# Optimization experiments

Hardware: AMD Instinct MI355X
Metric: run time of the kernel (lower is better)

Reference implementation:

```python
import jax, jax.numpy as jnp
import numpy as np

N = 2048
D = 1024
H = 16
DK = D // H
TOPK = 128
LN_EPS = 1e-5


def setup_inputs() -> dict:
    key = jax.random.key(0)
    ks = jax.random.split(key, 16)
    s = 1.0 / np.sqrt(D)
    sh = 1.0 / np.sqrt(H)
    return {
        "x": jax.random.normal(ks[0], (N, D), jnp.float32),
        "Wq": jax.random.normal(ks[1], (D, D), jnp.float32) * s,
        "bq": jnp.zeros((D,), jnp.float32),
        "Wk": jax.random.normal(ks[2], (D, D), jnp.float32) * s,
        "bk": jnp.zeros((D,), jnp.float32),
        "Wv": jax.random.normal(ks[3], (D, D), jnp.float32) * s,
        "bv": jnp.zeros((D,), jnp.float32),
        "Wpre": jax.random.normal(ks[4], (H, H), jnp.float32) * sh,
        "bpre": jnp.zeros((H,), jnp.float32),
        "Wpost": jax.random.normal(ks[5], (H, H), jnp.float32) * sh,
        "bpost": jnp.zeros((H,), jnp.float32),
        "Wo": jax.random.normal(ks[6], (D, D), jnp.float32) * s,
        "bo": jnp.zeros((D,), jnp.float32),
        "gamma": jnp.ones((D,), jnp.float32),
        "beta": jnp.zeros((D,), jnp.float32),
    }


def _layernorm(x, gamma, beta):
    mu = jnp.mean(x, axis=-1, keepdims=True)
    var = jnp.var(x, axis=-1, keepdims=True)
    return (x - mu) * jax.lax.rsqrt(var + LN_EPS) * gamma + beta


def reference(x, Wq, bq, Wk, bk, Wv, bv, Wpre, bpre, Wpost, bpost, Wo, bo, gamma, beta):
    n, d = x.shape
    residual = x
    xn = _layernorm(x, gamma, beta)
    # projections -> (n, H, dk)
    q = (xn @ Wq.T + bq).reshape(n, H, DK)
    k = (xn @ Wk.T + bk).reshape(n, H, DK)
    v = (xn @ Wv.T + bv).reshape(n, H, DK)
    scale = 1.0 / np.sqrt(float(DK))
    # full scores (H, n, n); torch chunking over q is math-equivalent (dropout=0)
    scores = jnp.einsum('qhd,khd->hqk', q, k) * scale
    # pre-softmax talking heads: mix over head axis (nn.Linear on last dim h)
    scores = jnp.einsum('hqk,gh->gqk', scores, Wpre) + bpre[:, None, None]
    attn = jax.nn.softmax(scores, axis=-1)
    # top-k sparsify + renormalize (threshold mask == torch scatter mask for distinct values)
    kth = jax.lax.top_k(attn, TOPK)[0][..., -1:]
    attn = jnp.where(attn >= kth, attn, 0.0)
    attn = attn / (jnp.sum(attn, axis=-1, keepdims=True) + 1e-9)
    # post-softmax talking heads
    attn = jnp.einsum('hqk,gh->gqk', attn, Wpost) + bpost[:, None, None]
    out = jnp.einsum('hqk,khd->qhd', attn, v).reshape(n, d)
    return residual + out @ Wo.T + bo
```

## Files before the change

### kernel.cpp

```cpp
#include <hip/hip_runtime.h>
#include <stdint.h>

typedef unsigned short u16;
using bf16x8 = __attribute__((ext_vector_type(8))) short;
using f32x4  = __attribute__((ext_vector_type(4))) float;

#define N_TOK 2048
#define DMODEL 1024
#define NHEAD 16
#define HDK 64
#define TOPK_K 128

__device__ __forceinline__ u16 f2b(float f) {
  unsigned u = __float_as_uint(f);
  return (u16)((u + 0x7FFFu + ((u >> 16) & 1u)) >> 16);
}
__device__ __forceinline__ float b2f(u16 b) {
  return __uint_as_float(((unsigned)b) << 16);
}
__device__ __forceinline__ float wave_reduce_sum(float v) {
#pragma unroll
  for (int d = 32; d >= 1; d >>= 1) v += __shfl_xor(v, d);
  return v;
}
__device__ __forceinline__ unsigned bits2key(unsigned u) {
  return (u & 0x80000000u) ? ~u : (u | 0x80000000u);
}
__device__ __forceinline__ float key2f(unsigned k) {
  unsigned u = (k & 0x80000000u) ? (k ^ 0x80000000u) : ~k;
  return __uint_as_float(u);
}

__global__ __launch_bounds__(256) void ln_kernel(const float* __restrict__ x,
                                                 const float* __restrict__ gamma,
                                                 const float* __restrict__ beta,
                                                 u16* __restrict__ xn) {
  int w = threadIdx.x >> 6, lane = threadIdx.x & 63;
  int row = blockIdx.x * 4 + w;
  const float4* xr = (const float4*)(x + (size_t)row * DMODEL);
  float4 v[4];
  float s = 0.f, ss = 0.f;
#pragma unroll
  for (int i = 0; i < 4; ++i) {
    v[i] = xr[i * 64 + lane];
    s += v[i].x + v[i].y + v[i].z + v[i].w;
    ss += v[i].x * v[i].x + v[i].y * v[i].y + v[i].z * v[i].z + v[i].w * v[i].w;
  }
  s = wave_reduce_sum(s);
  ss = wave_reduce_sum(ss);
  float mu = s * (1.f / DMODEL);
  float var = ss * (1.f / DMODEL) - mu * mu;
  float rstd = rsqrtf(var + 1e-5f);
  const float4* g4 = (const float4*)gamma;
  const float4* b4 = (const float4*)beta;
  u16* xo = xn + (size_t)row * DMODEL;
#pragma unroll
  for (int i = 0; i < 4; ++i) {
    float4 g = g4[i * 64 + lane], b = b4[i * 64 + lane];
    float ox = (v[i].x - mu) * rstd * g.x + b.x;
    float oy = (v[i].y - mu) * rstd * g.y + b.y;
    float oz = (v[i].z - mu) * rstd * g.z + b.z;
    float ow = (v[i].w - mu) * rstd * g.w + b.w;
    unsigned lo = (unsigned)f2b(ox) | ((unsigned)f2b(oy) << 16);
    unsigned hi = (unsigned)f2b(oz) | ((unsigned)f2b(ow) << 16);
    *(uint2*)&xo[(i * 64 + lane) * 4] = make_uint2(lo, hi);
  }
}

__global__ __launch_bounds__(256) void cast_kernel(const float* __restrict__ in,
                                                   u16* __restrict__ out, int n8) {
  int i = blockIdx.x * 256 + threadIdx.x;
  if (i >= n8) return;
  const float4* p = (const float4*)in + (size_t)i * 2;
  float4 a = p[0], b = p[1];
  unsigned w0 = (unsigned)f2b(a.x) | ((unsigned)f2b(a.y) << 16);
  unsigned w1 = (unsigned)f2b(a.z) | ((unsigned)f2b(a.w) << 16);
  unsigned w2 = (unsigned)f2b(b.x) | ((unsigned)f2b(b.y) << 16);
  unsigned w3 = (unsigned)f2b(b.z) | ((unsigned)f2b(b.w) << 16);
  *(uint4*)&out[(size_t)i * 8] = make_uint4(w0, w1, w2, w3);
}

__global__ __launch_bounds__(256) void concat3_kernel(const float* __restrict__ a,
                                                      const float* __restrict__ b,
                                                      const float* __restrict__ c,
                                                      float* __restrict__ out) {
  int i = blockIdx.x * 256 + threadIdx.x;
  if (i < 1024) out[i] = a[i];
  else if (i < 2048) out[i] = b[i - 1024];
  else if (i < 3072) out[i] = c[i - 2048];
}

__global__ __launch_bounds__(256) void transpose_kernel(const u16* __restrict__ V, int ldv,
                                                        u16* __restrict__ Vt) {
  __shared__ u16 tile[64][72];
  int kb = blockIdx.x * 64, cb = blockIdx.y * 64;
  int t = threadIdx.x;
  int r = t >> 2, cg = (t & 3) * 16;
  *(uint4*)&tile[r][cg]     = *(const uint4*)&V[(size_t)(kb + r) * ldv + cb + cg];
  *(uint4*)&tile[r][cg + 8] = *(const uint4*)&V[(size_t)(kb + r) * ldv + cb + cg + 8];
  __syncthreads();
  int c = t >> 2, kg = (t & 3) * 16;
  size_t base = (size_t)(cb + c) * N_TOK + kb + kg;
  unsigned p0 = (unsigned)tile[kg + 0][c] | ((unsigned)tile[kg + 1][c] << 16);
  unsigned p1 = (unsigned)tile[kg + 2][c] | ((unsigned)tile[kg + 3][c] << 16);
  unsigned p2 = (unsigned)tile[kg + 4][c] | ((unsigned)tile[kg + 5][c] << 16);
  unsigned p3 = (unsigned)tile[kg + 6][c] | ((unsigned)tile[kg + 7][c] << 16);
  unsigned p4 = (unsigned)tile[kg + 8][c] | ((unsigned)tile[kg + 9][c] << 16);
  unsigned p5 = (unsigned)tile[kg + 10][c] | ((unsigned)tile[kg + 11][c] << 16);
  unsigned p6 = (unsigned)tile[kg + 12][c] | ((unsigned)tile[kg + 13][c] << 16);
  unsigned p7 = (unsigned)tile[kg + 14][c] | ((unsigned)tile[kg + 15][c] << 16);
  *(uint4*)&Vt[base]     = make_uint4(p0, p1, p2, p3);
  *(uint4*)&Vt[base + 8] = make_uint4(p4, p5, p6, p7);
}

__global__ __launch_bounds__(256) void gemm_bf16_nt(
    const u16* __restrict__ A, int lda, int az,
    const u16* __restrict__ B, int ldb, int bz,
    void* __restrict__ Cv, int ldc, int cz,
    int K, float scale,
    const float* __restrict__ bias,
    const float* __restrict__ res, int out_f32) {
  __shared__ u16 As[64 * 40];
  __shared__ u16 Bs[64 * 40];
  A += (size_t)blockIdx.z * az;
  B += (size_t)blockIdx.z * bz;
  int bi = blockIdx.y * 64, bj = blockIdx.x * 64;
  int tid = threadIdx.x;
  int w = tid >> 6, lane = tid & 63;
  int wr = w >> 1, wc = w & 1;
  int lr = tid >> 2, lc = (tid & 3) * 8;
  int kh = (lane >> 4) * 8, fr = lane & 15;
  f32x4 acc[2][2] = {};
  for (int k0 = 0; k0 < K; k0 += 32) {
    *(uint4*)&As[lr * 40 + lc] = *(const uint4*)&A[(size_t)(bi + lr) * lda + k0 + lc];
    *(uint4*)&Bs[lr * 40 + lc] = *(const uint4*)&B[(size_t)(bj + lr) * ldb + k0 + lc];
    __syncthreads();
    bf16x8 a0 = *(bf16x8*)&As[(wr * 32 + fr) * 40 + kh];
    bf16x8 a1 = *(bf16x8*)&As[(wr * 32 + 16 + fr) * 40 + kh];
    bf16x8 b0 = *(bf16x8*)&Bs[(wc * 32 + fr) * 40 + kh];
    bf16x8 b1 = *(bf16x8*)&Bs[(wc * 32 + 16 + fr) * 40 + kh];
    acc[0][0] = __builtin_amdgcn_mfma_f32_16x16x32_bf16(a0, b0, acc[0][0], 0, 0, 0);
    acc[0][1] = __builtin_amdgcn_mfma_f32_16x16x32_bf16(a0, b1, acc[0][1], 0, 0, 0);
    acc[1][0] = __builtin_amdgcn_mfma_f32_16x16x32_bf16(a1, b0, acc[1][0], 0, 0, 0);
    acc[1][1] = __builtin_amdgcn_mfma_f32_16x16x32_bf16(a1, b1, acc[1][1], 0, 0, 0);
    __syncthreads();
  }
  float* Cf = (float*)Cv + (size_t)blockIdx.z * cz;
  u16* Ch = (u16*)Cv + (size_t)blockIdx.z * cz;
  int rg = (lane >> 4) * 4;
#pragma unroll
  for (int m = 0; m < 2; ++m) {
#pragma unroll
    for (int n = 0; n < 2; ++n) {
      int gcol = bj + wc * 32 + n * 16 + fr;
      float badd = bias ? bias[gcol] : 0.f;
#pragma unroll
      for (int r = 0; r < 4; ++r) {
        int grow = bi + wr * 32 + m * 16 + rg + r;
        size_t off = (size_t)grow * ldc + gcol;
        float v = acc[m][n][r] * scale + badd;
        if (res) v += res[off];
        if (out_f32) Cf[off] = v;
        else Ch[off] = f2b(v);
      }
    }
  }
}

__global__ __launch_bounds__(256) void headmix_kernel(
    const u16* __restrict__ in, const float* __restrict__ W,
    const float* __restrict__ bias, void* __restrict__ out, int out_f32) {
  __shared__ u16 tile[NHEAD][512];
  __shared__ float w_s[256];
  __shared__ float b_s[16];
  int q = blockIdx.x, kb = blockIdx.y * 512;
  int t = threadIdx.x;
  w_s[t] = W[t];
  if (t < 16) b_s[t] = bias ? bias[t] : 0.f;
#pragma unroll
  for (int j = 0; j < 4; ++j) {
    int idx = j * 256 + t;
    int h = idx >> 6, cu = idx & 63;
    ((uint4*)&tile[h][0])[cu] =
        ((const uint4*)(in + ((size_t)q * NHEAD + h) * N_TOK + kb))[cu];
  }
  __syncthreads();
  float sv0[16], sv1[16];
#pragma unroll
  for (int h = 0; h < 16; ++h) {
    unsigned pw = ((const unsigned*)&tile[h][0])[t];
    sv0[h] = b2f((u16)(pw & 0xFFFFu));
    sv1[h] = b2f((u16)(pw >> 16));
  }
#pragma unroll
  for (int g = 0; g < 16; ++g) {
    float a0 = b_s[g], a1 = b_s[g];
#pragma unroll
    for (int h = 0; h < 16; ++h) {
      float wv = w_s[g * 16 + h];
      a0 = fmaf(wv, sv0[h], a0);
      a1 = fmaf(wv, sv1[h], a1);
    }
    size_t obase = ((size_t)q * NHEAD + g) * N_TOK + kb;
    if (out_f32) {
      ((float2*)((float*)out + obase))[t] = make_float2(a0, a1);
    } else {
      ((unsigned*)((u16*)out + obase))[t] =
          (unsigned)f2b(a0) | ((unsigned)f2b(a1) << 16);
    }
  }
}

#define ACCS_APPLY(OP) \
  OP(0, A0.x, A0.y)  OP(1, A0.z, A0.w)  OP(2, A1.x, A1.y)  OP(3, A1.z, A1.w) \
  OP(4, A2.x, A2.y)  OP(5, A2.z, A2.w)  OP(6, A3.x, A3.y)  OP(7, A3.z, A3.w) \
  OP(8, A4.x, A4.y)  OP(9, A4.z, A4.w)  OP(10, A5.x, A5.y) OP(11, A5.z, A5.w) \
  OP(12, A6.x, A6.y) OP(13, A6.z, A6.w) OP(14, A7.x, A7.y) OP(15, A7.z, A7.w)
#define KEYS_APPLY(OP) \
  OP(Q0.x) OP(Q0.y) OP(Q0.z) OP(Q0.w) OP(Q1.x) OP(Q1.y) OP(Q1.z) OP(Q1.w) \
  OP(Q2.x) OP(Q2.y) OP(Q2.z) OP(Q2.w) OP(Q3.x) OP(Q3.y) OP(Q3.z) OP(Q3.w) \
  OP(Q4.x) OP(Q4.y) OP(Q4.z) OP(Q4.w) OP(Q5.x) OP(Q5.y) OP(Q5.z) OP(Q5.w) \
  OP(Q6.x) OP(Q6.y) OP(Q6.z) OP(Q6.w) OP(Q7.x) OP(Q7.y) OP(Q7.z) OP(Q7.w)

__global__ __launch_bounds__(256, 4) void premix_topk_kernel(
    const u16* __restrict__ Sin, const float* __restrict__ Wpre,
    u16* __restrict__ Sout) {
  int bid = blockIdx.x;
  int q = bid >> 2;
  int g = ((bid & 3) << 2) + (threadIdx.x >> 6);
  int lane = threadIdx.x & 63;
  const u16* slab = Sin + (size_t)q * (NHEAD * N_TOK);

  float4 A0 = {0,0,0,0}, A1 = {0,0,0,0}, A2 = {0,0,0,0}, A3 = {0,0,0,0};
  float4 A4 = {0,0,0,0}, A5 = {0,0,0,0}, A6 = {0,0,0,0}, A7 = {0,0,0,0};
#pragma unroll
  for (int h = 0; h < 16; ++h) {
    float wv = Wpre[g * 16 + h];
    const u16* rowp = slab + (size_t)h * N_TOK + 2 * lane;
#define PM(m, LO, HI) { unsigned pw = *(const unsigned*)(rowp + 128 * (m)); \
      LO = fmaf(wv, b2f((u16)(pw & 0xFFFFu)), LO); \
      HI = fmaf(wv, b2f((u16)(pw >> 16)), HI); }
    ACCS_APPLY(PM)
#undef PM
  }
  uint4 Q0, Q1, Q2, Q3, Q4, Q5, Q6, Q7;
  {
#define NK_IDX(F, AF) F = bits2key(__float_as_uint(AF));
    NK_IDX(Q0.x, A0.x) NK_IDX(Q0.y, A0.y) NK_IDX(Q0.z, A0.z) NK_IDX(Q0.w, A0.w)
    NK_IDX(Q1.x, A1.x) NK_IDX(Q1.y, A1.y) NK_IDX(Q1.z, A1.z) NK_IDX(Q1.w, A1.w)
    NK_IDX(Q2.x, A2.x) NK_IDX(Q2.y, A2.y) NK_IDX(Q2.z, A2.z) NK_IDX(Q2.w, A2.w)
    NK_IDX(Q3.x, A3.x) NK_IDX(Q3.y, A3.y) NK_IDX(Q3.z, A3.z) NK_IDX(Q3.w, A3.w)
    NK_IDX(Q4.x, A4.x) NK_IDX(Q4.y, A4.y) NK_IDX(Q4.z, A4.z) NK_IDX(Q4.w, A4.w)
    NK_IDX(Q5.x, A5.x) NK_IDX(Q5.y, A5.y) NK_IDX(Q5.z, A5.z) NK_IDX(Q5.w, A5.w)
    NK_IDX(Q6.x, A6.x) NK_IDX(Q6.y, A6.y) NK_IDX(Q6.z, A6.z) NK_IDX(Q6.w, A6.w)
    NK_IDX(Q7.x, A7.x) NK_IDX(Q7.y, A7.y) NK_IDX(Q7.z, A7.z) NK_IDX(Q7.w, A7.w)
#undef NK_IDX
  }
  unsigned kmax = 0u;
#define MX(KF) kmax = (KF) > kmax ? (KF) : kmax;
  KEYS_APPLY(MX)
#undef MX
#pragma unroll
  for (int d = 32; d >= 1; d >>= 1) {
    unsigned o = (unsigned)__shfl_xor((int)kmax, d);
    kmax = o > kmax ? o : kmax;
  }
  float mx = key2f(kmax);
  unsigned T = 0u;
#pragma unroll 1
  for (int bit = 31; bit >= 0; --bit) {
    unsigned cand = T | (1u << bit);
    int c = 0;
#define CNT(KF) c += (int)__popcll(__ballot((KF) >= cand));
    KEYS_APPLY(CNT)
#undef CNT
    if (c >= TOPK_K) T = cand;
    if (c == TOPK_K) break;
  }
  float z = 0.f, ms = 0.f;
#define ES(KF) { float ev = __expf(key2f(KF) - mx); z += ev; if ((KF) >= T) ms += ev; }
  KEYS_APPLY(ES)
#undef ES
  z = wave_reduce_sum(z);
  ms = wave_reduce_sum(ms);
  float cs = 1.f / (ms + 1e-9f * z);
  u16* op = Sout + ((size_t)q * NHEAD + g) * N_TOK + 2 * lane;
#define WB(m, LO, HI) { \
    float e0 = (LO >= T) ? __expf(key2f(LO) - mx) * cs : 0.f; \
    float e1 = (HI >= T) ? __expf(key2f(HI) - mx) * cs : 0.f; \
    *(unsigned*)(op + 128 * (m)) = (unsigned)f2b(e0) | ((unsigned)f2b(e1) << 16); }
  {
    uint4 A0 = Q0, A1 = Q1, A2 = Q2, A3 = Q3, A4 = Q4, A5 = Q5, A6 = Q6, A7 = Q7;
    ACCS_APPLY(WB)
  }
#undef WB
}

extern "C" void kernel_launch(void* const* d_in, const int* in_sizes, int n_in,
                              void* d_out, int out_size, void* d_ws, size_t ws_size,
                              hipStream_t stream) {
  const float* x     = (const float*)d_in[0];
  const float* Wq    = (const float*)d_in[1];
  const float* bq    = (const float*)d_in[2];
  const float* Wk    = (const float*)d_in[3];
  const float* bk    = (const float*)d_in[4];
  const float* Wv    = (const float*)d_in[5];
  const float* bv    = (const float*)d_in[6];
  const float* Wpre  = (const float*)d_in[7];
  const float* Wpost = (const float*)d_in[9];
  const float* bpost = (const float*)d_in[10];
  const float* Wo    = (const float*)d_in[11];
  const float* bo    = (const float*)d_in[12];
  const float* gamma = (const float*)d_in[13];
  const float* beta  = (const float*)d_in[14];

  const size_t NM = (size_t)N_TOK * DMODEL;
  const size_t WW = (size_t)DMODEL * DMODEL;
  const int D3 = 3 * DMODEL;
  char* p = (char*)d_ws;
  u16* xnb   = (u16*)p; p += NM * 2;
  u16* QKVb  = (u16*)p; p += (size_t)N_TOK * D3 * 2;
  u16* Vtb   = (u16*)p; p += NM * 2;
  u16* AOb   = (u16*)p; p += NM * 2;
  u16* WQKVb = (u16*)p; p += 3 * WW * 2;
  u16* Wob   = (u16*)p; p += WW * 2;
  float* bqkv = (float*)p; p += D3 * 4;
  size_t base = (size_t)(p - (char*)d_ws);

  int CQ = 0;
  const int cands[6] = {2048, 1024, 512, 256, 128, 64};
  for (int i = 0; i < 6; ++i) {
    size_t need = base + (size_t)cands[i] * NHEAD * N_TOK * 4;
    if (need <= ws_size) { CQ = cands[i]; break; }
  }
  if (CQ == 0) return;
  u16* Sa = (u16*)p;
  u16* Sb = (u16*)(p + (size_t)CQ * NHEAD * N_TOK * 2);

  ln_kernel<<<N_TOK / 4, 256, 0, stream>>>(x, gamma, beta, xnb);
  cast_kernel<<<512, 256, 0, stream>>>(Wq, WQKVb, WW / 8);
  cast_kernel<<<512, 256, 0, stream>>>(Wk, WQKVb + WW, WW / 8);
  cast_kernel<<<512, 256, 0, stream>>>(Wv, WQKVb + 2 * WW, WW / 8);
  cast_kernel<<<512, 256, 0, stream>>>(Wo, Wob, WW / 8);
  concat3_kernel<<<12, 256, 0, stream>>>(bq, bk, bv, bqkv);

  gemm_bf16_nt<<<dim3(48, 32, 1), 256, 0, stream>>>(xnb, DMODEL, 0, WQKVb, DMODEL, 0,
                                                    QKVb, D3, 0, DMODEL, 1.f, bqkv, nullptr, 0);
  transpose_kernel<<<dim3(N_TOK / 64, DMODEL / 64), 256, 0, stream>>>(QKVb + 2048, D3, Vtb);

  for (int q0 = 0; q0 < N_TOK; q0 += CQ) {
    gemm_bf16_nt<<<dim3(N_TOK / 64, CQ / 64, NHEAD), 256, 0, stream>>>(
        QKVb + (size_t)q0 * D3, D3, HDK, QKVb + 1024, D3, HDK,
        Sa, NHEAD * N_TOK, N_TOK, HDK, 0.125f, nullptr, nullptr, 0);

    premix_topk_kernel<<<CQ * 4, 256, 0, stream>>>(Sa, Wpre, Sb);

    headmix_kernel<<<dim3(CQ, 4), 256, 0, stream>>>(Sb, Wpost, bpost, Sb, 0);

    gemm_bf16_nt<<<dim3(1, CQ / 64, NHEAD), 256, 0, stream>>>(
        Sb, NHEAD * N_TOK, N_TOK, Vtb, N_TOK, HDK * N_TOK,
        AOb + (size_t)q0 * DMODEL, DMODEL, HDK, N_TOK, 1.f, nullptr, nullptr, 0);
  }

  gemm_bf16_nt<<<dim3(16, 32, 1), 256, 0, stream>>>(AOb, DMODEL, 0, Wob, DMODEL, 0,
                                                    d_out, DMODEL, 0, DMODEL, 1.f, bo, x, 1);
}
```

Measured before the change: 486.8 us.

## Fuse post-softmax head mixing into premix/top-k kernel via LDS

Merges the top-k softmax kernel and the post talking-heads mixing kernel into one block per query row of 1024 threads. The sparsified attention for all 16 heads is staged in shared memory, mixed over heads, and written back in place to a single score buffer. This removes a full global write and read of the attention tensor and one launch, and halves the score workspace. The cost is 64KB of LDS per block, which limits occupancy, and higher register pressure.

```diff
diff --git a/kernel.cpp b/kernel.cpp
--- a/kernel.cpp
+++ b/kernel.cpp
@@ -167,50 +167,6 @@
   }
 }
 
-__global__ __launch_bounds__(256) void headmix_kernel(
-    const u16* __restrict__ in, const float* __restrict__ W,
-    const float* __restrict__ bias, void* __restrict__ out, int out_f32) {
-  __shared__ u16 tile[NHEAD][512];
-  __shared__ float w_s[256];
-  __shared__ float b_s[16];
-  int q = blockIdx.x, kb = blockIdx.y * 512;
-  int t = threadIdx.x;
-  w_s[t] = W[t];
-  if (t < 16) b_s[t] = bias ? bias[t] : 0.f;
-#pragma unroll
-  for (int j = 0; j < 4; ++j) {
-    int idx = j * 256 + t;
-    int h = idx >> 6, cu = idx & 63;
-    ((uint4*)&tile[h][0])[cu] =
-        ((const uint4*)(in + ((size_t)q * NHEAD + h) * N_TOK + kb))[cu];
-  }
-  __syncthreads();
-  float sv0[16], sv1[16];
-#pragma unroll
-  for (int h = 0; h < 16; ++h) {
-    unsigned pw = ((const unsigned*)&tile[h][0])[t];
-    sv0[h] = b2f((u16)(pw & 0xFFFFu));
-    sv1[h] = b2f((u16)(pw >> 16));
-  }
-#pragma unroll
-  for (int g = 0; g < 16; ++g) {
-    float a0 = b_s[g], a1 = b_s[g];
-#pragma unroll
-    for (int h = 0; h < 16; ++h) {
-      float wv = w_s[g * 16 + h];
-      a0 = fmaf(wv, sv0[h], a0);
-      a1 = fmaf(wv, sv1[h], a1);
-    }
-    size_t obase = ((size_t)q * NHEAD + g) * N_TOK + kb;
-    if (out_f32) {
-      ((float2*)((float*)out + obase))[t] = make_float2(a0, a1);
-    } else {
-      ((unsigned*)((u16*)out + obase))[t] =
-          (unsigned)f2b(a0) | ((unsigned)f2b(a1) << 16);
-    }
-  }
-}
-
 #define ACCS_APPLY(OP) \
   OP(0, A0.x, A0.y)  OP(1, A0.z, A0.w)  OP(2, A1.x, A1.y)  OP(3, A1.z, A1.w) \
   OP(4, A2.x, A2.y)  OP(5, A2.z, A2.w)  OP(6, A3.x, A3.y)  OP(7, A3.z, A3.w) \
@@ -221,15 +177,24 @@
   OP(Q2.x) OP(Q2.y) OP(Q2.z) OP(Q2.w) OP(Q3.x) OP(Q3.y) OP(Q3.z) OP(Q3.w) \
   OP(Q4.x) OP(Q4.y) OP(Q4.z) OP(Q4.w) OP(Q5.x) OP(Q5.y) OP(Q5.z) OP(Q5.w) \
   OP(Q6.x) OP(Q6.y) OP(Q6.z) OP(Q6.w) OP(Q7.x) OP(Q7.y) OP(Q7.z) OP(Q7.w)
-
-__global__ __launch_bounds__(256, 4) void premix_topk_kernel(
-    const u16* __restrict__ Sin, const float* __restrict__ Wpre,
-    u16* __restrict__ Sout) {
-  int bid = blockIdx.x;
-  int q = bid >> 2;
-  int g = ((bid & 3) << 2) + (threadIdx.x >> 6);
+#define BACC_APPLY(OP) \
+  OP(0, B0.x, B0.y)  OP(1, B0.z, B0.w)  OP(2, B1.x, B1.y)  OP(3, B1.z, B1.w) \
+  OP(4, B2.x, B2.y)  OP(5, B2.z, B2.w)  OP(6, B3.x, B3.y)  OP(7, B3.z, B3.w) \
+  OP(8, B4.x, B4.y)  OP(9, B4.z, B4.w)  OP(10, B5.x, B5.y) OP(11, B5.z, B5.w) \
+  OP(12, B6.x, B6.y) OP(13, B6.z, B6.w) OP(14, B7.x, B7.y) OP(15, B7.z, B7.w)
+
+__global__ __launch_bounds__(1024, 4) void premix_topk_post_kernel(
+    u16* __restrict__ S, const float* __restrict__ Wpre,
+    const float* __restrict__ Wpost, const float* __restrict__ bpost) {
+  __shared__ u16 attn_lds[NHEAD][N_TOK];
+  __shared__ float w2_s[256], b2_s[16];
+  int q = blockIdx.x;
+  int g = threadIdx.x >> 6;
   int lane = threadIdx.x & 63;
-  const u16* slab = Sin + (size_t)q * (NHEAD * N_TOK);
+  int tid = threadIdx.x;
+  if (tid < 256) w2_s[tid] = Wpost[tid];
+  else if (tid < 272) b2_s[tid - 256] = bpost[tid - 256];
+  u16* slab = S + (size_t)q * (NHEAD * N_TOK);
 
   float4 A0 = {0,0,0,0}, A1 = {0,0,0,0}, A2 = {0,0,0,0}, A3 = {0,0,0,0};
   float4 A4 = {0,0,0,0}, A5 = {0,0,0,0}, A6 = {0,0,0,0}, A7 = {0,0,0,0};
@@ -284,16 +249,38 @@
   z = wave_reduce_sum(z);
   ms = wave_reduce_sum(ms);
   float cs = 1.f / (ms + 1e-9f * z);
-  u16* op = Sout + ((size_t)q * NHEAD + g) * N_TOK + 2 * lane;
+  u16* lp = &attn_lds[g][2 * lane];
 #define WB(m, LO, HI) { \
     float e0 = (LO >= T) ? __expf(key2f(LO) - mx) * cs : 0.f; \
     float e1 = (HI >= T) ? __expf(key2f(HI) - mx) * cs : 0.f; \
-    *(unsigned*)(op + 128 * (m)) = (unsigned)f2b(e0) | ((unsigned)f2b(e1) << 16); }
+    *(unsigned*)(lp + 128 * (m)) = (unsigned)f2b(e0) | ((unsigned)f2b(e1) << 16); }
   {
     uint4 A0 = Q0, A1 = Q1, A2 = Q2, A3 = Q3, A4 = Q4, A5 = Q5, A6 = Q6, A7 = Q7;
     ACCS_APPLY(WB)
   }
 #undef WB
+  __syncthreads();
+
+  int cb = g * 128 + 2 * lane;
+  float4 B0, B1, B2, B3, B4, B5, B6, B7;
+#define BI(gg, LO, HI) LO = b2_s[gg]; HI = b2_s[gg];
+  BACC_APPLY(BI)
+#undef BI
+#pragma unroll
+  for (int h = 0; h < 16; ++h) {
+    unsigned pw = *(const unsigned*)&attn_lds[h][cb];
+    float lo_ = b2f((u16)(pw & 0xFFFFu));
+    float hi_ = b2f((u16)(pw >> 16));
+#define BM(gg, LO, HI) { float wv = w2_s[(gg) * 16 + h]; \
+      LO = fmaf(wv, lo_, LO); HI = fmaf(wv, hi_, HI); }
+    BACC_APPLY(BM)
+#undef BM
+  }
+#define BW(gg, LO, HI) \
+  *(unsigned*)(slab + (size_t)(gg) * N_TOK + cb) = \
+      (unsigned)f2b(LO) | ((unsigned)f2b(HI) << 16);
+  BACC_APPLY(BW)
+#undef BW
 }
 
 extern "C" void kernel_launch(void* const* d_in, const int* in_sizes, int n_in,
@@ -330,12 +317,11 @@
   int CQ = 0;
   const int cands[6] = {2048, 1024, 512, 256, 128, 64};
   for (int i = 0; i < 6; ++i) {
-    size_t need = base + (size_t)cands[i] * NHEAD * N_TOK * 4;
+    size_t need = base + (size_t)cands[i] * NHEAD * N_TOK * 2;
     if (need <= ws_size) { CQ = cands[i]; break; }
   }
   if (CQ == 0) return;
-  u16* Sa = (u16*)p;
-  u16* Sb = (u16*)(p + (size_t)CQ * NHEAD * N_TOK * 2);
+  u16* S = (u16*)p;
 
   ln_kernel<<<N_TOK / 4, 256, 0, stream>>>(x, gamma, beta, xnb);
   cast_kernel<<<512, 256, 0, stream>>>(Wq, WQKVb, WW / 8);
@@ -351,14 +337,12 @@
   for (int q0 = 0; q0 < N_TOK; q0 += CQ) {
     gemm_bf16_nt<<<dim3(N_TOK / 64, CQ / 64, NHEAD), 256, 0, stream>>>(
         QKVb + (size_t)q0 * D3, D3, HDK, QKVb + 1024, D3, HDK,
-        Sa, NHEAD * N_TOK, N_TOK, HDK, 0.125f, nullptr, nullptr, 0);
-
-    premix_topk_kernel<<<CQ * 4, 256, 0, stream>>>(Sa, Wpre, Sb);
-
-    headmix_kernel<<<dim3(CQ, 4), 256, 0, stream>>>(Sb, Wpost, bpost, Sb, 0);
+        S, NHEAD * N_TOK, N_TOK, HDK, 0.125f, nullptr, nullptr, 0);
+
+    premix_topk_post_kernel<<<CQ, 1024, 0, stream>>>(S, Wpre, Wpost, bpost);
 
     gemm_bf16_nt<<<dim3(1, CQ / 64, NHEAD), 256, 0, stream>>>(
-        Sb, NHEAD * N_TOK, N_TOK, Vtb, N_TOK, HDK * N_TOK,
+        S, NHEAD * N_TOK, N_TOK, Vtb, N_TOK, HDK * N_TOK,
         AOb + (size_t)q0 * DMODEL, DMODEL, HDK, N_TOK, 1.f, nullptr, nullptr, 0);
   }
 
```

Measured after the change: 457.2 us. -6.1%, faster.
